# Kernel optimization log

Hardware: AMD Instinct MI355X
Metric: run time of the kernel (lower is better)

Reference implementation:

```python
import jax, jax.numpy as jnp
import numpy as np

TOP_K = 4
N_GROUP = 4
TOPK_GROUP = 2
ROUTED_SCALING = 1.0


def setup_inputs() -> dict:
    key = jax.random.key(0)
    k1, k2, k3, k4, k5 = jax.random.split(key, 5)
    B, S, H, I, E = 1, 2048, 1024, 512, 16
    hidden_states = jax.random.normal(k1, (B, S, H), dtype=jnp.float32)
    # router weight (kaiming-uniform-like scale)
    gate_weight = jax.random.normal(k2, (E, H), dtype=jnp.float32) * (1.0 / np.sqrt(H))
    e_bias = jnp.zeros((E,), dtype=jnp.float32)  # e_score_correction_bias buffer
    gate_proj = jax.random.normal(k3, (E, I, H), dtype=jnp.float32) * 0.02
    up_proj = jax.random.normal(k4, (E, I, H), dtype=jnp.float32) * 0.02
    down_proj = jax.random.normal(k5, (E, H, I), dtype=jnp.float32) * 0.02
    return {
        "hidden_states": hidden_states,
        "gate_weight": gate_weight,
        "e_bias": e_bias,
        "gate_proj": gate_proj,
        "up_proj": up_proj,
        "down_proj": down_proj,
    }


def _route(x_flat, gate_weight, e_bias):
    # x_flat: [T, H]
    T = x_flat.shape[0]
    E = gate_weight.shape[0]
    logits = jnp.einsum("th,eh->te", x_flat, gate_weight)
    scores = jax.nn.sigmoid(logits)                      # [T, E]
    scores_for_choice = scores + e_bias[None, :]
    # group scores = sum of top-2 expert scores within each group
    grp = scores_for_choice.reshape(T, N_GROUP, E // N_GROUP)
    top2, _ = jax.lax.top_k(grp, 2)
    group_scores = top2.sum(axis=-1)                     # [T, G]
    _, group_idx = jax.lax.top_k(group_scores, TOPK_GROUP)
    group_mask = jax.nn.one_hot(group_idx, N_GROUP, dtype=scores.dtype).sum(axis=1)  # [T, G]
    score_mask = jnp.repeat(group_mask, E // N_GROUP, axis=1)                        # [T, E]
    tmp_scores = jnp.where(score_mask > 0, scores_for_choice, 0.0)
    _, topk_idx = jax.lax.top_k(tmp_scores, TOP_K)       # [T, K]
    topk_weight = jnp.take_along_axis(scores, topk_idx, axis=1)
    denom = topk_weight.sum(axis=-1, keepdims=True) + 1e-20
    topk_weight = topk_weight / denom * ROUTED_SCALING
    return topk_idx, topk_weight


def reference(hidden_states, gate_weight, e_bias, gate_proj, up_proj, down_proj):
    B, S, H = hidden_states.shape
    E = gate_proj.shape[0]
    x = hidden_states.reshape(-1, H).astype(jnp.float32)  # [T, H]
    topk_idx, topk_weight = _route(x, gate_weight, e_bias)
    # combine weights per (token, expert): sum over the k slots selecting e
    combine = (jax.nn.one_hot(topk_idx, E, dtype=x.dtype) * topk_weight[..., None]).sum(axis=1)  # [T, E]
    # dense expert MLP (mathematically equal to gather-compute-scatter since
    # non-selected experts receive zero combine weight)
    g = jnp.einsum("th,eih->tei", x, gate_proj)
    u = jnp.einsum("th,eih->tei", x, up_proj)
    act = jax.nn.silu(g) * u                              # [T, E, I]
    expert_out = jnp.einsum("tei,ehi->teh", act, down_proj)
    y = jnp.einsum("teh,te->th", expert_out, combine)
    return y.reshape(B, S, H)
```

## Files before the change

### kernel.cpp

```cpp
#include <hip/hip_runtime.h>
#include <hip/hip_bf16.h>

typedef __attribute__((ext_vector_type(8))) short bf16x8;
typedef __attribute__((ext_vector_type(4))) float f32x4;

#define T_TOK 2048
#define HD 1024
#define ID 512
#define NE 16
#define TOPK 4
#define BK 64
#define WELEM (HD*ID*NE)

__device__ __forceinline__ unsigned pk2(float a, float b) {
    return __builtin_amdgcn_perm(__float_as_uint(b), __float_as_uint(a),
                                 0x07060302u);
}
__device__ __forceinline__ bf16x8 cvt8(const float* __restrict__ p) {
    float4 a = *(const float4*)p;
    float4 b = *(const float4*)(p + 4);
    union { bf16x8 v; unsigned u[4]; } r;
    r.u[0] = pk2(a.x, a.y); r.u[1] = pk2(a.z, a.w);
    r.u[2] = pk2(b.x, b.y); r.u[3] = pk2(b.z, b.w);
    return r.v;
}
__device__ __forceinline__ short f2bf(float f) {
    unsigned u = __float_as_uint(f);
    return (short)((u + 0x7fffu + ((u >> 16) & 1u)) >> 16);
}
__device__ __forceinline__ float bf2f(short s) {
    return __uint_as_float(((unsigned)(unsigned short)s) << 16);
}
__device__ __forceinline__ void load_lds16(const short* g, short* l) {
    __builtin_amdgcn_global_load_lds(
        (const __attribute__((address_space(1))) unsigned*)g,
        (__attribute__((address_space(3))) unsigned*)l, 16, 0, 0);
}

#define MFMA_BF16 __builtin_amdgcn_mfma_f32_16x16x32_bf16

__global__ __launch_bounds__(256) void conv_k(
        const float* __restrict__ s0, short* __restrict__ d0,
        const float* __restrict__ s1, short* __restrict__ d1,
        const float* __restrict__ s2, short* __restrict__ d2) {
    const float* src = (blockIdx.y == 0) ? s0 : (blockIdx.y == 1) ? s1 : s2;
    short* dst       = (blockIdx.y == 0) ? d0 : (blockIdx.y == 1) ? d1 : d2;
    size_t i = ((size_t)blockIdx.x * 256 + threadIdx.x) * 8;
    union { bf16x8 v; uint4 q; } r;
    r.v = cvt8(src + i);
    *(uint4*)(dst + i) = r.q;
}

__global__ __launch_bounds__(256) void router_k(
        const float* __restrict__ x, const float* __restrict__ gw,
        const float* __restrict__ eb,
        int* __restrict__ tk_idx, float* __restrict__ tk_w,
        short* __restrict__ xb) {
    int wid  = (blockIdx.x * 256 + threadIdx.x) >> 6;
    int lane = threadIdx.x & 63;

    const float* xr = x + (size_t)wid * HD + lane * 16;
    float xv[16];
#pragma unroll
    for (int c = 0; c < 4; c++) {
        float4 v = *(const float4*)(xr + c * 4);
        xv[4 * c] = v.x; xv[4 * c + 1] = v.y; xv[4 * c + 2] = v.z; xv[4 * c + 3] = v.w;
    }
    {
        union { uint4 q; unsigned u[4]; } w0, w1;
        w0.u[0] = pk2(xv[0], xv[1]);  w0.u[1] = pk2(xv[2], xv[3]);
        w0.u[2] = pk2(xv[4], xv[5]);  w0.u[3] = pk2(xv[6], xv[7]);
        w1.u[0] = pk2(xv[8], xv[9]);  w1.u[1] = pk2(xv[10], xv[11]);
        w1.u[2] = pk2(xv[12], xv[13]); w1.u[3] = pk2(xv[14], xv[15]);
        short* d = xb + ((size_t)wid << 10) + lane * 16;
        *(uint4*)d = w0.q;
        *(uint4*)(d + 8) = w1.q;
    }

    float logits[NE];
#pragma unroll
    for (int e = 0; e < NE; e++) {
        const float* gr = gw + e * HD + lane * 16;
        float p = 0.f;
#pragma unroll
        for (int c = 0; c < 4; c++) {
            float4 v = *(const float4*)(gr + c * 4);
            p += xv[4 * c] * v.x + xv[4 * c + 1] * v.y +
                 xv[4 * c + 2] * v.z + xv[4 * c + 3] * v.w;
        }
#pragma unroll
        for (int s = 32; s > 0; s >>= 1) p += __shfl_xor(p, s, 64);
        logits[e] = p;
    }

    float scores[NE], sc[NE];
#pragma unroll
    for (int e = 0; e < NE; e++) {
        scores[e] = 1.f / (1.f + __expf(-logits[e]));
        sc[e] = scores[e] + eb[e];
    }

    float gs[4];
#pragma unroll
    for (int g = 0; g < 4; g++) {
        float a = sc[4 * g], b = sc[4 * g + 1], c = sc[4 * g + 2], d = sc[4 * g + 3];
        float h1 = fmaxf(a, b), l1 = fminf(a, b);
        float h2 = fmaxf(c, d), l2 = fminf(c, d);
        gs[g] = fmaxf(h1, h2) + fmaxf(fminf(h1, h2), fmaxf(l1, l2));
    }
    int g0 = 0; float b0 = gs[0];
#pragma unroll
    for (int g = 1; g < 4; g++) if (gs[g] > b0) { b0 = gs[g]; g0 = g; }
    int g1 = -1; float b1 = -1e30f;
#pragma unroll
    for (int g = 0; g < 4; g++) if (g != g0 && gs[g] > b1) { b1 = gs[g]; g1 = g; }

    int taken = 0;
    int bid[TOPK]; float bsc[TOPK]; float wsum = 0.f;
#pragma unroll
    for (int k = 0; k < TOPK; k++) {
        float bv = -1e30f; int bi = 0; float bs = 0.f;
#pragma unroll
        for (int e = 0; e < NE; e++) {
            int grp = e >> 2;
            bool ok = ((grp == g0) || (grp == g1)) && !((taken >> e) & 1);
            if (ok && sc[e] > bv) { bv = sc[e]; bi = e; bs = scores[e]; }
        }
        taken |= (1 << bi);
        bid[k] = bi; bsc[k] = bs; wsum += bs;
    }
    if (lane == 0) {
        float inv = 1.0f / (wsum + 1e-20f);
#pragma unroll
        for (int k = 0; k < TOPK; k++) {
            tk_idx[wid * TOPK + k] = bid[k];
            tk_w[wid * TOPK + k]   = bsc[k] * inv;
        }
    }
}

__global__ __launch_bounds__(256) void assign_k(
        const int* __restrict__ tk_idx,
        int* __restrict__ counts, int* __restrict__ tok_list,
        int* __restrict__ pair_slot) {
    int p = blockIdx.x * 256 + threadIdx.x;
    int e = tk_idx[p];
    int slot = atomicAdd(&counts[e], 1);
    tok_list[e * T_TOK + slot] = p >> 2;
    pair_slot[p] = slot;
}

__global__ void offs_k(const int* __restrict__ counts, int* __restrict__ offs) {
    if (threadIdx.x == 0) {
        int a = 0;
#pragma unroll
        for (int e = 0; e < NE; e++) { offs[e] = a; a += counts[e]; }
    }
}

__global__ __launch_bounds__(256) void gemm1_k(
        const short* __restrict__ xb,
        const short* __restrict__ gpb,
        const short* __restrict__ upb,
        const int* __restrict__ counts,
        const int* __restrict__ offs,
        const int* __restrict__ tok_list,
        short* __restrict__ act) {
    __shared__ short xs[2][128 * BK];
    __shared__ short gs[2][64 * BK];
    __shared__ short us[2][64 * BK];
    __shared__ int   tok_s[128];

    int e = blockIdx.z;
    int cnt = counts[e];
    int base = blockIdx.y * 128;
    if (base >= cnt) return;
    int arow0 = offs[e] + base;

    int tid = threadIdx.x;
    if (tid < 128) {
        int s = base + tid;
        tok_s[tid] = (s < cnt) ? tok_list[e * T_TOK + s] : tok_list[e * T_TOK];
    }
    __syncthreads();

    int wv = tid >> 6, lane = tid & 63;
    int qd = lane >> 4, l16 = lane & 15;
    int wm = (wv >> 1) * 64, wn = (wv & 1) * 32;
    int nb0 = blockIdx.x * 64;
    const short* gp = gpb + (size_t)e * ID * HD + (size_t)nb0 * HD;
    const short* up = upb + (size_t)e * ID * HD + (size_t)nb0 * HD;

    const short* xsg[4]; short* xld[4];
#pragma unroll
    for (int i = 0; i < 4; i++) {
        int idx = i * 256 + tid, r = idx >> 3, c = idx & 7;
        xsg[i] = xb + ((size_t)tok_s[r] << 10) + (((c ^ r) & 7) << 3);
        xld[i] = &xs[0][(i * 256 + wv * 64) * 8];
    }
    const short* gsg[2]; const short* usg[2]; short* gld[2]; short* uld[2];
#pragma unroll
    for (int i = 0; i < 2; i++) {
        int idx = i * 256 + tid, r = idx >> 3, c = idx & 7;
        size_t so = (size_t)r * HD + (((c ^ r) & 7) << 3);
        gsg[i] = gp + so;
        usg[i] = up + so;
        gld[i] = &gs[0][(i * 256 + wv * 64) * 8];
        uld[i] = &us[0][(i * 256 + wv * 64) * 8];
    }

    f32x4 accg[4][2] = {};
    f32x4 accu[4][2] = {};

    auto STAGE = [&](int kp, int b) {
#pragma unroll
        for (int i = 0; i < 4; i++)
            load_lds16(xsg[i] + kp, xld[i] + b * (128 * BK));
#pragma unroll
        for (int i = 0; i < 2; i++) {
            load_lds16(gsg[i] + kp, gld[i] + b * (64 * BK));
            load_lds16(usg[i] + kp, uld[i] + b * (64 * BK));
        }
    };
    auto COMPUTE = [&](int b) {
        const short* xsb = xs[b];
        const short* gsb = gs[b];
        const short* usb = us[b];
#pragma unroll
        for (int ks = 0; ks < 2; ks++) {
            int cb = ks * 4 + qd;
            bf16x8 af[4], bg[2], bu[2];
#pragma unroll
            for (int i = 0; i < 4; i++) {
                int r = wm + i * 16 + l16;
                af[i] = *(const bf16x8*)&xsb[(r << 6) + (((cb ^ r) & 7) << 3)];
            }
#pragma unroll
            for (int j = 0; j < 2; j++) {
                int r = wn + j * 16 + l16;
                int lo = (r << 6) + (((cb ^ r) & 7) << 3);
                bg[j] = *(const bf16x8*)&gsb[lo];
                bu[j] = *(const bf16x8*)&usb[lo];
            }
#pragma unroll
            for (int i = 0; i < 4; i++)
#pragma unroll
                for (int j = 0; j < 2; j++) {
                    accg[i][j] = MFMA_BF16(af[i], bg[j], accg[i][j], 0, 0, 0);
                    accu[i][j] = MFMA_BF16(af[i], bu[j], accu[i][j], 0, 0, 0);
                }
        }
    };

    constexpr int NP = HD / BK;
    STAGE(0, 0);
    auto STEP = [&](int p, int b) {
        if (p + 1 < NP) {
            STAGE((p + 1) * BK, b ^ 1);
            asm volatile("s_waitcnt vmcnt(8)" ::: "memory");
        } else {
            asm volatile("s_waitcnt vmcnt(0)" ::: "memory");
        }
        __builtin_amdgcn_s_barrier();
        asm volatile("" ::: "memory");
        COMPUTE(b);
        asm volatile("" ::: "memory");
        __builtin_amdgcn_s_barrier();
    };
#pragma unroll 1
    for (int p = 0; p < NP; p += 2) { STEP(p, 0); STEP(p + 1, 1); }

#pragma unroll
    for (int i = 0; i < 4; i++)
#pragma unroll
        for (int j = 0; j < 2; j++)
#pragma unroll
            for (int r = 0; r < 4; r++) {
                int m = wm + i * 16 + qd * 4 + r;
                if (base + m < cnt) {
                    float g = accg[i][j][r], u = accu[i][j][r];
                    float a = g / (1.f + __expf(-g)) * u;
                    act[(size_t)(arow0 + m) * ID + nb0 + wn + j * 16 + l16] = f2bf(a);
                }
            }
}

__global__ __launch_bounds__(256) void gemm2_k(
        const short* __restrict__ act,
        const short* __restrict__ dpb,
        const int* __restrict__ counts,
        const int* __restrict__ offs,
        short* __restrict__ yexp) {
    __shared__ short as_[2][128 * BK];
    __shared__ short ds_[2][128 * BK];

    int e = blockIdx.z;
    int cnt = counts[e];
    int base = blockIdx.y * 128;
    if (base >= cnt) return;
    int arow0 = offs[e] + base;

    int tid = threadIdx.x;
    int wv = tid >> 6, lane = tid & 63;
    int qd = lane >> 4, l16 = lane & 15;
    int wm = (wv >> 1) * 64, wn = (wv & 1) * 64;
    int hb0 = blockIdx.x * 128;
    const short* dp = dpb + (size_t)e * HD * ID + (size_t)hb0 * ID;

    const short* asg[4]; const short* dsg[4]; short* ald[4]; short* dld[4];
#pragma unroll
    for (int i = 0; i < 4; i++) {
        int idx = i * 256 + tid, r = idx >> 3, c = idx & 7;
        int sw = ((c ^ r) & 7) << 3;
        asg[i] = act + (size_t)(arow0 + r) * ID + sw;
        dsg[i] = dp + (size_t)r * ID + sw;
        ald[i] = &as_[0][(i * 256 + wv * 64) * 8];
        dld[i] = &ds_[0][(i * 256 + wv * 64) * 8];
    }

    f32x4 acc[4][4] = {};

    auto STAGE = [&](int kp, int b) {
#pragma unroll
        for (int i = 0; i < 4; i++) {
            load_lds16(asg[i] + kp, ald[i] + b * (128 * BK));
            load_lds16(dsg[i] + kp, dld[i] + b * (128 * BK));
        }
    };
    auto COMPUTE = [&](int b) {
        const short* asb = as_[b];
        const short* dsb = ds_[b];
#pragma unroll
        for (int ks = 0; ks < 2; ks++) {
            int cb = ks * 4 + qd;
            bf16x8 af[4], bd[4];
#pragma unroll
            for (int i = 0; i < 4; i++) {
                int r = wm + i * 16 + l16;
                af[i] = *(const bf16x8*)&asb[(r << 6) + (((cb ^ r) & 7) << 3)];
                int r2 = wn + i * 16 + l16;
                bd[i] = *(const bf16x8*)&dsb[(r2 << 6) + (((cb ^ r2) & 7) << 3)];
            }
#pragma unroll
            for (int i = 0; i < 4; i++)
#pragma unroll
                for (int j = 0; j < 4; j++)
                    acc[i][j] = MFMA_BF16(af[i], bd[j], acc[i][j], 0, 0, 0);
        }
    };

    constexpr int NP = ID / BK;
    STAGE(0, 0);
    auto STEP = [&](int p, int b) {
        if (p + 1 < NP) {
            STAGE((p + 1) * BK, b ^ 1);
            asm volatile("s_waitcnt vmcnt(8)" ::: "memory");
        } else {
            asm volatile("s_waitcnt vmcnt(0)" ::: "memory");
        }
        __builtin_amdgcn_s_barrier();
        asm volatile("" ::: "memory");
        COMPUTE(b);
        asm volatile("" ::: "memory");
        __builtin_amdgcn_s_barrier();
    };
#pragma unroll 1
    for (int p = 0; p < NP; p += 2) { STEP(p, 0); STEP(p + 1, 1); }

#pragma unroll
    for (int i = 0; i < 4; i++)
#pragma unroll
        for (int j = 0; j < 4; j++)
#pragma unroll
            for (int r = 0; r < 4; r++) {
                int m = wm + i * 16 + qd * 4 + r;
                if (base + m < cnt)
                    yexp[(size_t)(arow0 + m) * HD + hb0 + wn + j * 16 + l16] =
                        f2bf(acc[i][j][r]);
            }
}

__global__ __launch_bounds__(256) void combine_k(
        const short* __restrict__ yexp,
        const int* __restrict__ offs,
        const int* __restrict__ tk_idx, const float* __restrict__ tk_w,
        const int* __restrict__ pair_slot,
        float* __restrict__ out) {
    int t = blockIdx.x * 2 + (threadIdx.x >> 7);
    int i = threadIdx.x & 127;
    float acc[8] = {};
#pragma unroll
    for (int k = 0; k < TOPK; k++) {
        int p = t * TOPK + k;
        int e = tk_idx[p];
        int row = offs[e] + pair_slot[p];
        float w = tk_w[p];
        bf16x8 v = *(const bf16x8*)(yexp + (size_t)row * HD + i * 8);
#pragma unroll
        for (int j = 0; j < 8; j++) acc[j] += w * bf2f(v[j]);
    }
    float4 o0 = {acc[0], acc[1], acc[2], acc[3]};
    float4 o1 = {acc[4], acc[5], acc[6], acc[7]};
    float* d = out + (size_t)t * HD + i * 8;
    *(float4*)d = o0;
    *(float4*)(d + 4) = o1;
}

extern "C" void kernel_launch(void* const* d_in, const int* in_sizes, int n_in,
                              void* d_out, int out_size, void* d_ws, size_t ws_size,
                              hipStream_t stream) {
    const float* x  = (const float*)d_in[0];
    const float* gw = (const float*)d_in[1];
    const float* eb = (const float*)d_in[2];
    const float* gp = (const float*)d_in[3];
    const float* up = (const float*)d_in[4];
    const float* dp = (const float*)d_in[5];

    short* gpb = (short*)d_ws;
    short* upb = gpb + WELEM;
    short* dpb = upb + WELEM;
    short* xb  = dpb + WELEM;
    short* act = xb + (size_t)T_TOK * HD;
    int* counts    = (int*)(act + (size_t)(T_TOK * TOPK + 128) * ID);
    int* offs      = counts + NE;
    int* tok_list  = offs + NE;
    int* pair_slot = tok_list + NE * T_TOK;
    int* tk_idx    = pair_slot + T_TOK * TOPK;
    float* tk_w    = (float*)(tk_idx + T_TOK * TOPK);
    short* yexp = gpb;

    hipMemsetAsync(counts, 0, NE * sizeof(int), stream);

    conv_k<<<dim3(WELEM / 8 / 256, 3), 256, 0, stream>>>(gp, gpb, up, upb,
                                                         dp, dpb);
    router_k<<<T_TOK / 4, 256, 0, stream>>>(x, gw, eb, tk_idx, tk_w, xb);
    assign_k<<<T_TOK * TOPK / 256, 256, 0, stream>>>(tk_idx, counts,
                                                     tok_list, pair_slot);
    offs_k<<<1, 64, 0, stream>>>(counts, offs);
    gemm1_k<<<dim3(ID / 64, T_TOK / 128, NE), 256, 0, stream>>>(
        xb, gpb, upb, counts, offs, tok_list, act);
    gemm2_k<<<dim3(HD / 128, T_TOK / 128, NE), 256, 0, stream>>>(
        act, dpb, counts, offs, yexp);
    combine_k<<<T_TOK / 2, 256, 0, stream>>>(yexp, offs, tk_idx, tk_w,
                                             pair_slot, (float*)d_out);
}
```

Before: 246.3 us.

## Fuse routing bookkeeping into router, deepen GEMM pipeline, reorder grid by expert

Removes the memset, assign and offset kernels by zeroing counts in the conversion kernel, doing the slot atomics inside the router, and recomputing expert offsets in each consumer. Both expert GEMMs switch from a two-stage BK=64 pipeline to a four-stage BK=32 pipeline with a new 4-way swizzle. The grid is reordered so the expert index is the fastest-varying block dimension. This cuts launch overhead and aims to hide more load latency, at the cost of more barriers per K and redundant offset sums in every block.

New measurement: 322.6 us. 1.31x slower.

```diff
diff --git a/kernel.cpp b/kernel.cpp
--- a/kernel.cpp
+++ b/kernel.cpp
@@ -9,7 +9,7 @@
 #define ID 512
 #define NE 16
 #define TOPK 4
-#define BK 64
+#define BK 32
 #define WELEM (HD*ID*NE)
 
 __device__ __forceinline__ unsigned pk2(float a, float b) {
@@ -42,7 +42,10 @@
 __global__ __launch_bounds__(256) void conv_k(
         const float* __restrict__ s0, short* __restrict__ d0,
         const float* __restrict__ s1, short* __restrict__ d1,
-        const float* __restrict__ s2, short* __restrict__ d2) {
+        const float* __restrict__ s2, short* __restrict__ d2,
+        int* __restrict__ counts) {
+    if (blockIdx.x == 0 && blockIdx.y == 0 && threadIdx.x < NE)
+        counts[threadIdx.x] = 0;
     const float* src = (blockIdx.y == 0) ? s0 : (blockIdx.y == 1) ? s1 : s2;
     short* dst       = (blockIdx.y == 0) ? d0 : (blockIdx.y == 1) ? d1 : d2;
     size_t i = ((size_t)blockIdx.x * 256 + threadIdx.x) * 8;
@@ -55,7 +58,9 @@
         const float* __restrict__ x, const float* __restrict__ gw,
         const float* __restrict__ eb,
         int* __restrict__ tk_idx, float* __restrict__ tk_w,
-        short* __restrict__ xb) {
+        short* __restrict__ xb,
+        int* __restrict__ counts, int* __restrict__ tok_list,
+        int* __restrict__ pair_slot) {
     int wid  = (blockIdx.x * 256 + threadIdx.x) >> 6;
     int lane = threadIdx.x & 63;
 
@@ -133,28 +138,13 @@
         float inv = 1.0f / (wsum + 1e-20f);
 #pragma unroll
         for (int k = 0; k < TOPK; k++) {
-            tk_idx[wid * TOPK + k] = bid[k];
+            int ee = bid[k];
+            int slot = atomicAdd(&counts[ee], 1);
+            tok_list[ee * T_TOK + slot] = wid;
+            pair_slot[wid * TOPK + k] = slot;
+            tk_idx[wid * TOPK + k] = ee;
             tk_w[wid * TOPK + k]   = bsc[k] * inv;
         }
-    }
-}
-
-__global__ __launch_bounds__(256) void assign_k(
-        const int* __restrict__ tk_idx,
-        int* __restrict__ counts, int* __restrict__ tok_list,
-        int* __restrict__ pair_slot) {
-    int p = blockIdx.x * 256 + threadIdx.x;
-    int e = tk_idx[p];
-    int slot = atomicAdd(&counts[e], 1);
-    tok_list[e * T_TOK + slot] = p >> 2;
-    pair_slot[p] = slot;
-}
-
-__global__ void offs_k(const int* __restrict__ counts, int* __restrict__ offs) {
-    if (threadIdx.x == 0) {
-        int a = 0;
-#pragma unroll
-        for (int e = 0; e < NE; e++) { offs[e] = a; a += counts[e]; }
     }
 }
 
@@ -163,19 +153,20 @@
         const short* __restrict__ gpb,
         const short* __restrict__ upb,
         const int* __restrict__ counts,
-        const int* __restrict__ offs,
         const int* __restrict__ tok_list,
         short* __restrict__ act) {
-    __shared__ short xs[2][128 * BK];
-    __shared__ short gs[2][64 * BK];
-    __shared__ short us[2][64 * BK];
+    __shared__ short xs[4][128 * BK];
+    __shared__ short gs[4][64 * BK];
+    __shared__ short us[4][64 * BK];
     __shared__ int   tok_s[128];
 
-    int e = blockIdx.z;
+    int e = blockIdx.x;
     int cnt = counts[e];
-    int base = blockIdx.y * 128;
+    int base = blockIdx.z * 128;
     if (base >= cnt) return;
-    int arow0 = offs[e] + base;
+    int off = 0;
+    for (int q = 0; q < NE; q++) if (q < e) off += counts[q];
+    int arow0 = off + base;
 
     int tid = threadIdx.x;
     if (tid < 128) {
@@ -187,77 +178,73 @@
     int wv = tid >> 6, lane = tid & 63;
     int qd = lane >> 4, l16 = lane & 15;
     int wm = (wv >> 1) * 64, wn = (wv & 1) * 32;
-    int nb0 = blockIdx.x * 64;
+    int nb0 = blockIdx.y * 64;
     const short* gp = gpb + (size_t)e * ID * HD + (size_t)nb0 * HD;
     const short* up = upb + (size_t)e * ID * HD + (size_t)nb0 * HD;
 
-    const short* xsg[4]; short* xld[4];
-#pragma unroll
-    for (int i = 0; i < 4; i++) {
-        int idx = i * 256 + tid, r = idx >> 3, c = idx & 7;
-        xsg[i] = xb + ((size_t)tok_s[r] << 10) + (((c ^ r) & 7) << 3);
-        xld[i] = &xs[0][(i * 256 + wv * 64) * 8];
-    }
-    const short* gsg[2]; const short* usg[2]; short* gld[2]; short* uld[2];
+    const short* xsg[2]; int xo[2];
 #pragma unroll
     for (int i = 0; i < 2; i++) {
-        int idx = i * 256 + tid, r = idx >> 3, c = idx & 7;
-        size_t so = (size_t)r * HD + (((c ^ r) & 7) << 3);
-        gsg[i] = gp + so;
-        usg[i] = up + so;
-        gld[i] = &gs[0][(i * 256 + wv * 64) * 8];
-        uld[i] = &us[0][(i * 256 + wv * 64) * 8];
+        int idx = i * 256 + tid, r = idx >> 2, s = idx & 3;
+        int rr = (r ^ (r >> 2)) & 3;
+        xsg[i] = xb + ((size_t)tok_s[r] << 10) + ((s ^ rr) << 3);
+        xo[i] = (i * 256 + wv * 64) * 8;
+    }
+    const short* gsg; const short* usg; int guo;
+    {
+        int r = tid >> 2, s = tid & 3;
+        int rr = (r ^ (r >> 2)) & 3;
+        size_t so = (size_t)r * HD + ((s ^ rr) << 3);
+        gsg = gp + so;
+        usg = up + so;
+        guo = (wv * 64) * 8;
     }
 
     f32x4 accg[4][2] = {};
     f32x4 accu[4][2] = {};
 
     auto STAGE = [&](int kp, int b) {
+        load_lds16(xsg[0] + kp, &xs[b][xo[0]]);
+        load_lds16(xsg[1] + kp, &xs[b][xo[1]]);
+        load_lds16(gsg + kp, &gs[b][guo]);
+        load_lds16(usg + kp, &us[b][guo]);
+    };
+    auto COMPUTE = [&](int b) {
+        int cb = qd;
+        bf16x8 af[4], bg[2], bu[2];
+#pragma unroll
+        for (int i = 0; i < 4; i++) {
+            int r = wm + i * 16 + l16;
+            int sl = (cb ^ r ^ (r >> 2)) & 3;
+            af[i] = *(const bf16x8*)&xs[b][r * BK + sl * 8];
+        }
+#pragma unroll
+        for (int j = 0; j < 2; j++) {
+            int r = wn + j * 16 + l16;
+            int sl = (cb ^ r ^ (r >> 2)) & 3;
+            int lo = r * BK + sl * 8;
+            bg[j] = *(const bf16x8*)&gs[b][lo];
+            bu[j] = *(const bf16x8*)&us[b][lo];
+        }
 #pragma unroll
         for (int i = 0; i < 4; i++)
-            load_lds16(xsg[i] + kp, xld[i] + b * (128 * BK));
-#pragma unroll
-        for (int i = 0; i < 2; i++) {
-            load_lds16(gsg[i] + kp, gld[i] + b * (64 * BK));
-            load_lds16(usg[i] + kp, uld[i] + b * (64 * BK));
-        }
-    };
-    auto COMPUTE = [&](int b) {
-        const short* xsb = xs[b];
-        const short* gsb = gs[b];
-        const short* usb = us[b];
-#pragma unroll
-        for (int ks = 0; ks < 2; ks++) {
-            int cb = ks * 4 + qd;
-            bf16x8 af[4], bg[2], bu[2];
-#pragma unroll
-            for (int i = 0; i < 4; i++) {
-                int r = wm + i * 16 + l16;
-                af[i] = *(const bf16x8*)&xsb[(r << 6) + (((cb ^ r) & 7) << 3)];
+#pragma unroll
+            for (int j = 0; j < 2; j++) {
+                accg[i][j] = MFMA_BF16(af[i], bg[j], accg[i][j], 0, 0, 0);
+                accu[i][j] = MFMA_BF16(af[i], bu[j], accu[i][j], 0, 0, 0);
             }
-#pragma unroll
-            for (int j = 0; j < 2; j++) {
-                int r = wn + j * 16 + l16;
-                int lo = (r << 6) + (((cb ^ r) & 7) << 3);
-                bg[j] = *(const bf16x8*)&gsb[lo];
-                bu[j] = *(const bf16x8*)&usb[lo];
-            }
-#pragma unroll
-            for (int i = 0; i < 4; i++)
-#pragma unroll
-                for (int j = 0; j < 2; j++) {
-                    accg[i][j] = MFMA_BF16(af[i], bg[j], accg[i][j], 0, 0, 0);
-                    accu[i][j] = MFMA_BF16(af[i], bu[j], accu[i][j], 0, 0, 0);
-                }
-        }
     };
 
     constexpr int NP = HD / BK;
-    STAGE(0, 0);
+    STAGE(0, 0); STAGE(BK, 1); STAGE(2 * BK, 2);
     auto STEP = [&](int p, int b) {
-        if (p + 1 < NP) {
-            STAGE((p + 1) * BK, b ^ 1);
+        if (p + 3 < NP) {
+            STAGE((p + 3) * BK, (b + 3) & 3);
+            asm volatile("s_waitcnt vmcnt(12)" ::: "memory");
+        } else if (p + 3 == NP) {
             asm volatile("s_waitcnt vmcnt(8)" ::: "memory");
+        } else if (p + 2 == NP) {
+            asm volatile("s_waitcnt vmcnt(4)" ::: "memory");
         } else {
             asm volatile("s_waitcnt vmcnt(0)" ::: "memory");
         }
@@ -268,7 +255,9 @@
         __builtin_amdgcn_s_barrier();
     };
 #pragma unroll 1
-    for (int p = 0; p < NP; p += 2) { STEP(p, 0); STEP(p + 1, 1); }
+    for (int p = 0; p < NP; p += 4) {
+        STEP(p, 0); STEP(p + 1, 1); STEP(p + 2, 2); STEP(p + 3, 3);
+    }
 
 #pragma unroll
     for (int i = 0; i < 4; i++)
@@ -289,72 +278,73 @@
         const short* __restrict__ act,
         const short* __restrict__ dpb,
         const int* __restrict__ counts,
-        const int* __restrict__ offs,
         short* __restrict__ yexp) {
-    __shared__ short as_[2][128 * BK];
-    __shared__ short ds_[2][128 * BK];
-
-    int e = blockIdx.z;
+    __shared__ short as_[4][128 * BK];
+    __shared__ short ds_[4][128 * BK];
+
+    int e = blockIdx.x;
     int cnt = counts[e];
-    int base = blockIdx.y * 128;
+    int base = blockIdx.z * 128;
     if (base >= cnt) return;
-    int arow0 = offs[e] + base;
+    int off = 0;
+    for (int q = 0; q < NE; q++) if (q < e) off += counts[q];
+    int arow0 = off + base;
 
     int tid = threadIdx.x;
     int wv = tid >> 6, lane = tid & 63;
     int qd = lane >> 4, l16 = lane & 15;
     int wm = (wv >> 1) * 64, wn = (wv & 1) * 64;
-    int hb0 = blockIdx.x * 128;
+    int hb0 = blockIdx.y * 128;
     const short* dp = dpb + (size_t)e * HD * ID + (size_t)hb0 * ID;
 
-    const short* asg[4]; const short* dsg[4]; short* ald[4]; short* dld[4];
-#pragma unroll
-    for (int i = 0; i < 4; i++) {
-        int idx = i * 256 + tid, r = idx >> 3, c = idx & 7;
-        int sw = ((c ^ r) & 7) << 3;
+    const short* asg[2]; const short* dsg[2]; int ao[2];
+#pragma unroll
+    for (int i = 0; i < 2; i++) {
+        int idx = i * 256 + tid, r = idx >> 2, s = idx & 3;
+        int rr = (r ^ (r >> 2)) & 3;
+        int sw = (s ^ rr) << 3;
         asg[i] = act + (size_t)(arow0 + r) * ID + sw;
         dsg[i] = dp + (size_t)r * ID + sw;
-        ald[i] = &as_[0][(i * 256 + wv * 64) * 8];
-        dld[i] = &ds_[0][(i * 256 + wv * 64) * 8];
+        ao[i] = (i * 256 + wv * 64) * 8;
     }
 
     f32x4 acc[4][4] = {};
 
     auto STAGE = [&](int kp, int b) {
+        load_lds16(asg[0] + kp, &as_[b][ao[0]]);
+        load_lds16(asg[1] + kp, &as_[b][ao[1]]);
+        load_lds16(dsg[0] + kp, &ds_[b][ao[0]]);
+        load_lds16(dsg[1] + kp, &ds_[b][ao[1]]);
+    };
+    auto COMPUTE = [&](int b) {
+        int cb = qd;
+        bf16x8 af[4], bd[4];
 #pragma unroll
         for (int i = 0; i < 4; i++) {
-            load_lds16(asg[i] + kp, ald[i] + b * (128 * BK));
-            load_lds16(dsg[i] + kp, dld[i] + b * (128 * BK));
-        }
-    };
-    auto COMPUTE = [&](int b) {
-        const short* asb = as_[b];
-        const short* dsb = ds_[b];
-#pragma unroll
-        for (int ks = 0; ks < 2; ks++) {
-            int cb = ks * 4 + qd;
-            bf16x8 af[4], bd[4];
-#pragma unroll
-            for (int i = 0; i < 4; i++) {
-                int r = wm + i * 16 + l16;
-                af[i] = *(const bf16x8*)&asb[(r << 6) + (((cb ^ r) & 7) << 3)];
-                int r2 = wn + i * 16 + l16;
-                bd[i] = *(const bf16x8*)&dsb[(r2 << 6) + (((cb ^ r2) & 7) << 3)];
-            }
-#pragma unroll
-            for (int i = 0; i < 4; i++)
-#pragma unroll
-                for (int j = 0; j < 4; j++)
-                    acc[i][j] = MFMA_BF16(af[i], bd[j], acc[i][j], 0, 0, 0);
-        }
+            int r = wm + i * 16 + l16;
+            int sl = (cb ^ r ^ (r >> 2)) & 3;
+            af[i] = *(const bf16x8*)&as_[b][r * BK + sl * 8];
+            int r2 = wn + i * 16 + l16;
+            int sl2 = (cb ^ r2 ^ (r2 >> 2)) & 3;
+            bd[i] = *(const bf16x8*)&ds_[b][r2 * BK + sl2 * 8];
+        }
+#pragma unroll
+        for (int i = 0; i < 4; i++)
+#pragma unroll
+            for (int j = 0; j < 4; j++)
+                acc[i][j] = MFMA_BF16(af[i], bd[j], acc[i][j], 0, 0, 0);
     };
 
     constexpr int NP = ID / BK;
-    STAGE(0, 0);
+    STAGE(0, 0); STAGE(BK, 1); STAGE(2 * BK, 2);
     auto STEP = [&](int p, int b) {
-        if (p + 1 < NP) {
-            STAGE((p + 1) * BK, b ^ 1);
+        if (p + 3 < NP) {
+            STAGE((p + 3) * BK, (b + 3) & 3);
+            asm volatile("s_waitcnt vmcnt(12)" ::: "memory");
+        } else if (p + 3 == NP) {
             asm volatile("s_waitcnt vmcnt(8)" ::: "memory");
+        } else if (p + 2 == NP) {
+            asm volatile("s_waitcnt vmcnt(4)" ::: "memory");
         } else {
             asm volatile("s_waitcnt vmcnt(0)" ::: "memory");
         }
@@ -365,7 +355,9 @@
         __builtin_amdgcn_s_barrier();
     };
 #pragma unroll 1
-    for (int p = 0; p < NP; p += 2) { STEP(p, 0); STEP(p + 1, 1); }
+    for (int p = 0; p < NP; p += 4) {
+        STEP(p, 0); STEP(p + 1, 1); STEP(p + 2, 2); STEP(p + 3, 3);
+    }
 
 #pragma unroll
     for (int i = 0; i < 4; i++)
@@ -382,10 +374,18 @@
 
 __global__ __launch_bounds__(256) void combine_k(
         const short* __restrict__ yexp,
-        const int* __restrict__ offs,
+        const int* __restrict__ counts,
         const int* __restrict__ tk_idx, const float* __restrict__ tk_w,
         const int* __restrict__ pair_slot,
         float* __restrict__ out) {
+    __shared__ int offs_s[NE];
+    if (threadIdx.x == 0) {
+        int a = 0;
+#pragma unroll
+        for (int e = 0; e < NE; e++) { offs_s[e] = a; a += counts[e]; }
+    }
+    __syncthreads();
+
     int t = blockIdx.x * 2 + (threadIdx.x >> 7);
     int i = threadIdx.x & 127;
     float acc[8] = {};
@@ -393,7 +393,7 @@
     for (int k = 0; k < TOPK; k++) {
         int p = t * TOPK + k;
         int e = tk_idx[p];
-        int row = offs[e] + pair_slot[p];
+        int row = offs_s[e] + pair_slot[p];
         float w = tk_w[p];
         bf16x8 v = *(const bf16x8*)(yexp + (size_t)row * HD + i * 8);
 #pragma unroll
@@ -422,25 +422,20 @@
     short* xb  = dpb + WELEM;
     short* act = xb + (size_t)T_TOK * HD;
     int* counts    = (int*)(act + (size_t)(T_TOK * TOPK + 128) * ID);
-    int* offs      = counts + NE;
-    int* tok_list  = offs + NE;
+    int* tok_list  = counts + NE;
     int* pair_slot = tok_list + NE * T_TOK;
     int* tk_idx    = pair_slot + T_TOK * TOPK;
     float* tk_w    = (float*)(tk_idx + T_TOK * TOPK);
     short* yexp = gpb;
 
-    hipMemsetAsync(counts, 0, NE * sizeof(int), stream);
-
     conv_k<<<dim3(WELEM / 8 / 256, 3), 256, 0, stream>>>(gp, gpb, up, upb,
-                                                         dp, dpb);
-    router_k<<<T_TOK / 4, 256, 0, stream>>>(x, gw, eb, tk_idx, tk_w, xb);
-    assign_k<<<T_TOK * TOPK / 256, 256, 0, stream>>>(tk_idx, counts,
-                                                     tok_list, pair_slot);
-    offs_k<<<1, 64, 0, stream>>>(counts, offs);
-    gemm1_k<<<dim3(ID / 64, T_TOK / 128, NE), 256, 0, stream>>>(
-        xb, gpb, upb, counts, offs, tok_list, act);
-    gemm2_k<<<dim3(HD / 128, T_TOK / 128, NE), 256, 0, stream>>>(
-        act, dpb, counts, offs, yexp);
-    combine_k<<<T_TOK / 2, 256, 0, stream>>>(yexp, offs, tk_idx, tk_w,
+                                                         dp, dpb, counts);
+    router_k<<<T_TOK / 4, 256, 0, stream>>>(x, gw, eb, tk_idx, tk_w, xb,
+                                            counts, tok_list, pair_slot);
+    gemm1_k<<<dim3(NE, ID / 64, T_TOK / 128), 256, 0, stream>>>(
+        xb, gpb, upb, counts, tok_list, act);
+    gemm2_k<<<dim3(NE, HD / 128, T_TOK / 128), 256, 0, stream>>>(
+        act, dpb, counts, yexp);
+    combine_k<<<T_TOK / 2, 256, 0, stream>>>(yexp, counts, tk_idx, tk_w,
                                              pair_slot, (float*)d_out);
 }
```
